# Optimization experiments

Hardware: AMD Instinct MI355X
Metric: run time of the kernel (lower is better)

The kernel has to match this reference:

```python
import jax, jax.numpy as jnp
import numpy as np

B, S, H = 2, 2048, 4096
NH, NKV, HD = 32, 8, 128
Q_SIZE, KV_SIZE = NH * HD, NKV * HD
ROPE_THETA = 10000.0


def setup_inputs() -> dict:
    key = jax.random.key(0)
    k1, k2, k3 = jax.random.split(key, 3)
    positions = jnp.tile(jnp.arange(S, dtype=jnp.int64 if jax.config.jax_enable_x64 else jnp.int32), (B, 1))
    hidden_states = jax.random.normal(k1, (B, S, H), dtype=jnp.float32)
    w_qkv = jax.random.normal(k2, (H, Q_SIZE + 2 * KV_SIZE), dtype=jnp.float32) * 0.02
    w_o = jax.random.normal(k3, (Q_SIZE, H), dtype=jnp.float32) * 0.02
    return {"positions": positions, "hidden_states": hidden_states, "w_qkv": w_qkv, "w_o": w_o}


def _apply_rope(x, positions):
    # x: [B, S, nheads, HD]; neox-style rotate-half RoPE
    half = HD // 2
    inv_freq = 1.0 / (ROPE_THETA ** (jnp.arange(0, half, dtype=jnp.float32) / half))
    freqs = positions.astype(jnp.float32)[..., None] * inv_freq  # [B, S, HD/2]
    cos = jnp.cos(freqs)[:, :, None, :]  # [B, S, 1, HD/2]
    sin = jnp.sin(freqs)[:, :, None, :]
    x1, x2 = x[..., :half], x[..., half:]
    return jnp.concatenate([x1 * cos - x2 * sin, x2 * cos + x1 * sin], axis=-1)


def reference(positions, hidden_states, w_qkv, w_o):
    qkv = jnp.einsum("bsh,hd->bsd", hidden_states, w_qkv)
    q = qkv[..., :Q_SIZE].reshape(B, S, NH, HD)
    k = qkv[..., Q_SIZE:Q_SIZE + KV_SIZE].reshape(B, S, NKV, HD)
    v = qkv[..., Q_SIZE + KV_SIZE:].reshape(B, S, NKV, HD)

    q = _apply_rope(q, positions)
    k = _apply_rope(k, positions)

    # GQA: expand kv heads to match query heads
    rep = NH // NKV
    k = jnp.repeat(k, rep, axis=2)  # [B, S, NH, HD]
    v = jnp.repeat(v, rep, axis=2)

    scale = 1.0 / jnp.sqrt(jnp.float32(HD))
    scores = jnp.einsum("bqhd,bkhd->bhqk", q, k) * scale  # [B, NH, S, S]
    causal = jnp.tril(jnp.ones((S, S), dtype=bool))
    scores = jnp.where(causal[None, None], scores, jnp.finfo(scores.dtype).min)
    probs = jax.nn.softmax(scores, axis=-1)

    attn = jnp.einsum("bhqk,bkhd->bqhd", probs, v).reshape(B, S, Q_SIZE)
    return jnp.einsum("bsd,dh->bsh", attn, w_o)
```

## Files before the change

### kernel.cpp

```cpp
#include <hip/hip_runtime.h>
#include <hip/hip_bf16.h>
#include <math.h>


typedef __attribute__((ext_vector_type(8))) __bf16 bf16x8;
typedef __attribute__((ext_vector_type(4))) float floatx4;

__device__ __forceinline__ floatx4 mfma16(bf16x8 a, bf16x8 b, floatx4 c) {
    return __builtin_amdgcn_mfma_f32_16x16x32_bf16(a, b, c, 0, 0, 0);
}

__device__ __forceinline__ void load_lds16(const __hip_bfloat16* g,
                                           __hip_bfloat16* lds_base_uniform) {
    __builtin_amdgcn_global_load_lds(
        (const __attribute__((address_space(1))) unsigned int*)g,
        (__attribute__((address_space(3))) unsigned int*)lds_base_uniform,
        16, 0, 0);
}

__global__ __launch_bounds__(256)
void convert_kernel(const float* __restrict__ in, __hip_bfloat16* __restrict__ out,
                    int n) {
    int i = (blockIdx.x * 256 + threadIdx.x) * 4;
    if (i >= n) return;
    float4 v = *(const float4*)(in + i);
    union { __hip_bfloat16 h[4]; uint2 u; } pk;
    pk.h[0] = __float2bfloat16(v.x);
    pk.h[1] = __float2bfloat16(v.y);
    pk.h[2] = __float2bfloat16(v.z);
    pk.h[3] = __float2bfloat16(v.w);
    *(uint2*)(out + i) = pk.u;
}

__global__ __launch_bounds__(256)
void transpose_f32_bf16_kernel(const float* __restrict__ in,
                               __hip_bfloat16* __restrict__ out, int R, int C) {
    __shared__ __hip_bfloat16 tile[64][65];
    const int r0 = blockIdx.y * 64, c0 = blockIdx.x * 64;
    const int t = threadIdx.x;
    #pragma unroll
    for (int i = 0; i < 16; ++i) {
        int idx = t + 256 * i;
        int rl = idx >> 6, cl = idx & 63;
        tile[rl][cl] = __float2bfloat16(in[(size_t)(r0 + rl) * C + (c0 + cl)]);
    }
    __syncthreads();
    #pragma unroll
    for (int i = 0; i < 16; ++i) {
        int idx = t + 256 * i;
        int cl = idx >> 6, rl = idx & 63;
        out[(size_t)(c0 + cl) * R + (r0 + rl)] = tile[rl][cl];
    }
}

__global__ __launch_bounds__(256)
void transpose_bf16_kernel(const __hip_bfloat16* __restrict__ in,
                           __hip_bfloat16* __restrict__ out, int R, int C) {
    __shared__ __hip_bfloat16 tile[64][65];
    const int bz = blockIdx.z;
    const __hip_bfloat16* inb  = in  + (size_t)bz * R * C;
    __hip_bfloat16*       outb = out + (size_t)bz * R * C;
    const int r0 = blockIdx.y * 64, c0 = blockIdx.x * 64;
    const int t = threadIdx.x;
    #pragma unroll
    for (int i = 0; i < 16; ++i) {
        int idx = t + 256 * i;
        int rl = idx >> 6, cl = idx & 63;
        tile[rl][cl] = inb[(size_t)(r0 + rl) * C + (c0 + cl)];
    }
    __syncthreads();
    #pragma unroll
    for (int i = 0; i < 16; ++i) {
        int idx = t + 256 * i;
        int cl = idx >> 6, rl = idx & 63;
        outb[(size_t)(c0 + cl) * R + (r0 + rl)] = tile[rl][cl];
    }
}

template <int MODE>
__global__ __launch_bounds__(256)
void gemm_bt_kernel(const __hip_bfloat16* __restrict__ A,
                    const __hip_bfloat16* __restrict__ Bt,
                    float* __restrict__ Cp,
                    __hip_bfloat16* __restrict__ Qr,
                    __hip_bfloat16* __restrict__ Kr,
                    __hip_bfloat16* __restrict__ Vv,
                    int M, int N, int K) {
    __shared__ __align__(16) __hip_bfloat16 As[128 * 32];
    __shared__ __align__(16) __hip_bfloat16 Bs[128 * 32];

    const int m0 = blockIdx.y * 128, n0 = blockIdx.x * 128;
    const int tid  = threadIdx.x;
    const int wave = tid >> 6, lane = tid & 63;
    const int quad = lane >> 4, l16 = lane & 15;
    const int wm = (wave >> 1) * 64, wn = (wave & 1) * 64;

    floatx4 acc[4][4] = {};

    for (int kt = 0; kt < K; kt += 32) {
        #pragma unroll
        for (int i = 0; i < 2; ++i) {
            int idx = tid + 256 * i;
            int row = idx >> 2;
            int kc  = (idx & 3) << 3;
            __hip_bfloat16* dstA = &As[(size_t)(wave * 64 + 256 * i) * 8];
            __hip_bfloat16* dstB = &Bs[(size_t)(wave * 64 + 256 * i) * 8];
            load_lds16(&A [(size_t)(m0 + row) * K + kt + kc], dstA);
            load_lds16(&Bt[(size_t)(n0 + row) * K + kt + kc], dstB);
        }
        __syncthreads();

        bf16x8 af[4], bfv[4];
        #pragma unroll
        for (int i = 0; i < 4; ++i)
            af[i]  = *(const bf16x8*)(&As[(wm + i * 16 + l16) * 32 + quad * 8]);
        #pragma unroll
        for (int j = 0; j < 4; ++j)
            bfv[j] = *(const bf16x8*)(&Bs[(wn + j * 16 + l16) * 32 + quad * 8]);
        #pragma unroll
        for (int i = 0; i < 4; ++i)
            #pragma unroll
            for (int j = 0; j < 4; ++j)
                acc[i][j] = mfma16(af[i], bfv[j], acc[i][j]);
        __syncthreads();
    }

    #pragma unroll
    for (int i = 0; i < 4; ++i) {
        #pragma unroll
        for (int j = 0; j < 4; ++j) {
            int col = n0 + wn + j * 16 + l16;
            #pragma unroll
            for (int r = 0; r < 4; ++r) {
                int row = m0 + wm + i * 16 + quad * 4 + r;
                if (MODE == 0) {
                    Cp[(size_t)row * N + col] = acc[i][j][r];
                } else {
                    __hip_bfloat16 v = __float2bfloat16(acc[i][j][r]);
                    int bb = row >> 11, s = row & 2047;
                    int d  = col & 127;
                    if (col < 4096) {
                        int h = col >> 7;
                        Qr[(((size_t)bb * 32 + h) * 2048 + s) * 128 + d] = v;
                    } else if (col < 5120) {
                        int kvh = (col - 4096) >> 7;
                        Kr[(((size_t)bb * 8 + kvh) * 2048 + s) * 128 + d] = v;
                    } else {
                        int kvh = (col - 5120) >> 7;
                        Vv[(((size_t)bb * 8 + kvh) * 2048 + s) * 128 + d] = v;
                    }
                }
            }
        }
    }
}

__global__ __launch_bounds__(256)
void rope_kernel(__hip_bfloat16* __restrict__ x,
                 const int* __restrict__ positions, int nrows, int bshift,
                 float qscale) {
    int gid = blockIdx.x * 256 + threadIdx.x;
    if (gid >= nrows * 64) return;
    int row = gid >> 6, d = gid & 63;
    int s = row & 2047;
    int b = row >> bshift;
    float p = (float)positions[(b << 11) + s];
    float ang = p * expf(-0.14391156831212787f * (float)d);
    float sn, cs;
    sincosf(ang, &sn, &cs);
    __hip_bfloat16* ptr = x + (size_t)row * 128;
    float x1 = __bfloat162float(ptr[d]);
    float x2 = __bfloat162float(ptr[d + 64]);
    ptr[d]      = __float2bfloat16((x1 * cs - x2 * sn) * qscale);
    ptr[d + 64] = __float2bfloat16((x2 * cs + x1 * sn) * qscale);
}

__global__ __launch_bounds__(256)
void attn_kernel(const __hip_bfloat16* __restrict__ Qr,
                 const __hip_bfloat16* __restrict__ Kr,
                 const __hip_bfloat16* __restrict__ Vt,
                 __hip_bfloat16* __restrict__ Ao) {
    __shared__ __align__(16) __hip_bfloat16 Ks[32 * 136];
    __shared__ __align__(16) __hip_bfloat16 Vs[128 * 36];
    __shared__ __align__(16) __hip_bfloat16 Pl[4][32 * 40];

    const int tid  = threadIdx.x;
    const int wave = tid >> 6, lane = tid & 63;
    const int quad = lane >> 4, l16 = lane & 15;
    const int qb = (gridDim.x - 1) - blockIdx.x;
    const int q0 = qb * 128;
    const int qr0 = q0 + wave * 32;
    const int h  = blockIdx.y;
    const int b  = blockIdx.z;
    const int kv = h >> 2;

    const __hip_bfloat16* Qb = Qr + ((size_t)b * 32 + h)  * 2048 * 128;
    const __hip_bfloat16* Kb = Kr + ((size_t)b * 8  + kv) * 2048 * 128;
    const __hip_bfloat16* Vb = Vt + ((size_t)b * 8  + kv) * 128 * 2048;

    bf16x8 qf[2][4];
    #pragma unroll
    for (int i = 0; i < 2; ++i)
        #pragma unroll
        for (int kc = 0; kc < 4; ++kc)
            qf[i][kc] = *(const bf16x8*)(
                &Qb[(size_t)(qr0 + i * 16 + l16) * 128 + kc * 32 + quad * 8]);

    float m_i[2][4];
    #pragma unroll
    for (int i = 0; i < 2; ++i)
        #pragma unroll
        for (int r = 0; r < 4; ++r) m_i[i][r] = -1e30f;
    floatx4 o[2][8] = {};
    floatx4 lsum[2] = {};

    bf16x8 ones;
    #pragma unroll
    for (int e = 0; e < 8; ++e) ones[e] = (__bf16)1.0f;

    const int kmax = q0 + 127;

    for (int ks = 0; ks <= kmax; ks += 32) {
        #pragma unroll
        for (int p = 0; p < 2; ++p) {
            int idx = tid + 256 * p;
            int krow = idx >> 4, kcol = (idx & 15) << 3;
            *(uint4*)(&Ks[krow * 136 + kcol]) =
                *(const uint4*)(&Kb[(size_t)(ks + krow) * 128 + kcol]);
        }
        #pragma unroll
        for (int p = 0; p < 2; ++p) {
            int idx = tid + 256 * p;
            int d = idx >> 2, koff = (idx & 3) << 3;
            *(uint4*)(&Vs[d * 36 + koff]) =
                *(const uint4*)(&Vb[(size_t)d * 2048 + ks + koff]);
        }
        __syncthreads();

        if (ks <= qr0 + 31) {
            const bool fullt = (ks + 31 <= qr0);

            floatx4 sacc[2][2] = {};
            __builtin_amdgcn_s_setprio(1);
            #pragma unroll
            for (int j = 0; j < 2; ++j) {
                #pragma unroll
                for (int kc = 0; kc < 4; ++kc) {
                    bf16x8 kf = *(const bf16x8*)(
                        &Ks[(j * 16 + l16) * 136 + kc * 32 + quad * 8]);
                    #pragma unroll
                    for (int i = 0; i < 2; ++i)
                        sacc[i][j] = mfma16(qf[i][kc], kf, sacc[i][j]);
                }
            }
            __builtin_amdgcn_s_setprio(0);

            #pragma unroll
            for (int i = 0; i < 2; ++i) {
                #pragma unroll
                for (int r = 0; r < 4; ++r) {
                    int row = qr0 + i * 16 + quad * 4 + r;
                    float s0 = sacc[i][0][r];
                    float s1 = sacc[i][1][r];
                    if (!fullt) {
                        if (ks + l16 > row)      s0 = -1e30f;
                        if (ks + 16 + l16 > row) s1 = -1e30f;
                    }
                    float mx = fmaxf(s0, s1);
                    #pragma unroll
                    for (int off = 1; off < 16; off <<= 1)
                        mx = fmaxf(mx, __shfl_xor(mx, off, 64));
                    float mnew = fmaxf(m_i[i][r], mx);
                    float a  = __expf(m_i[i][r] - mnew);
                    float p0 = __expf(s0 - mnew);
                    float p1 = __expf(s1 - mnew);
                    Pl[wave][(i * 16 + quad * 4 + r) * 40 + l16]      =
                        __float2bfloat16(p0);
                    Pl[wave][(i * 16 + quad * 4 + r) * 40 + 16 + l16] =
                        __float2bfloat16(p1);
                    m_i[i][r] = mnew;
                    lsum[i][r] *= a;
                    #pragma unroll
                    for (int dn = 0; dn < 8; ++dn)
                        o[i][dn][r] *= a;
                }
            }

            bf16x8 pf[2];
            #pragma unroll
            for (int i = 0; i < 2; ++i)
                pf[i] = *(const bf16x8*)(&Pl[wave][(i * 16 + l16) * 40 + quad * 8]);

            __builtin_amdgcn_s_setprio(1);
            #pragma unroll
            for (int i = 0; i < 2; ++i)
                lsum[i] = mfma16(pf[i], ones, lsum[i]);
            #pragma unroll
            for (int dn = 0; dn < 8; ++dn) {
                bf16x8 vf = *(const bf16x8*)(
                    &Vs[(dn * 16 + l16) * 36 + quad * 8]);
                #pragma unroll
                for (int i = 0; i < 2; ++i)
                    o[i][dn] = mfma16(pf[i], vf, o[i][dn]);
            }
            __builtin_amdgcn_s_setprio(0);
        }
        __syncthreads();
    }

    #pragma unroll
    for (int i = 0; i < 2; ++i) {
        #pragma unroll
        for (int r = 0; r < 4; ++r) {
            float inv = 1.0f / lsum[i][r];
            int row = qr0 + i * 16 + quad * 4 + r;
            size_t base = ((size_t)b * 2048 + row) * 4096 + (size_t)h * 128;
            #pragma unroll
            for (int dn = 0; dn < 8; ++dn)
                Ao[base + dn * 16 + l16] = __float2bfloat16(o[i][dn][r] * inv);
        }
    }
}

extern "C" void kernel_launch(void* const* d_in, const int* in_sizes, int n_in,
                              void* d_out, int out_size, void* d_ws, size_t ws_size,
                              hipStream_t stream) {
    const int*   positions = (const int*)d_in[0];
    const float* hidden    = (const float*)d_in[1];
    const float* wqkv      = (const float*)d_in[2];
    const float* wo        = (const float*)d_in[3];
    float* out = (float*)d_out;

    __hip_bfloat16* WqkvT = (__hip_bfloat16*)d_ws;
    __hip_bfloat16* WoT   = WqkvT + 25165824;
    __hip_bfloat16* Hb    = WoT   + 16777216;
    __hip_bfloat16* Qr    = Hb    + 16777216;
    __hip_bfloat16* Kr    = Qr    + 16777216;
    __hip_bfloat16* Vv    = Kr    + 4194304;
    __hip_bfloat16* Ao    = WqkvT;
    __hip_bfloat16* Vt    = Hb;

    convert_kernel<<<16777216 / 1024, 256, 0, stream>>>(hidden, Hb, 16777216);
    transpose_f32_bf16_kernel<<<dim3(6144 / 64, 4096 / 64), 256, 0, stream>>>(
        wqkv, WqkvT, 4096, 6144);
    transpose_f32_bf16_kernel<<<dim3(4096 / 64, 4096 / 64), 256, 0, stream>>>(
        wo, WoT, 4096, 4096);

    gemm_bt_kernel<1><<<dim3(6144 / 128, 4096 / 128), 256, 0, stream>>>(
        Hb, WqkvT, nullptr, Qr, Kr, Vv, 4096, 6144, 4096);

    rope_kernel<<<(131072 * 64) / 256, 256, 0, stream>>>(
        Qr, positions, 131072, 16, 0.08838834764831845f);
    rope_kernel<<<(32768  * 64) / 256, 256, 0, stream>>>(
        Kr, positions, 32768, 14, 1.0f);

    transpose_bf16_kernel<<<dim3(128 / 64, 2048 / 64, 16), 256, 0, stream>>>(
        Vv, Vt, 2048, 128);

    attn_kernel<<<dim3(2048 / 128, 32, 2), 256, 0, stream>>>(Qr, Kr, Vt, Ao);

    gemm_bt_kernel<0><<<dim3(4096 / 128, 4096 / 128), 256, 0, stream>>>(
        Ao, WoT, out, nullptr, nullptr, nullptr, 4096, 4096, 4096);
}
```

Measured before the change: 1.082 ms.

## Double-buffer K/V tiles via async global-to-LDS loads with XOR swizzle

The attention kernel now stages K and V tiles into two LDS buffers using direct global_load_lds, prefetching the next tile while the current one is computed. This replaces the synchronous register round-trip and the barrier before each tile. Padding is swapped for XOR swizzles on K, V and P to avoid LDS bank conflicts. Query-block ordering is also alternated across heads to balance the causal workload. The change relies on a single barrier per iteration being enough to order the async LDS writes against reads of the other buffer.

```diff
diff --git a/kernel.cpp b/kernel.cpp
--- a/kernel.cpp
+++ b/kernel.cpp
@@ -175,19 +175,37 @@
     ptr[d + 64] = __float2bfloat16((x2 * cs + x1 * sn) * qscale);
 }
 
+__device__ __forceinline__ void stage_tiles(const __hip_bfloat16* __restrict__ Kb,
+                                            const __hip_bfloat16* __restrict__ Vb,
+                                            int ks,
+                                            __hip_bfloat16* KsBuf,
+                                            __hip_bfloat16* VsBuf,
+                                            int tid, int wave) {
+    #pragma unroll
+    for (int p = 0; p < 2; ++p) {
+        int idx  = tid + 256 * p;
+        int krow = idx >> 4, kc16 = idx & 15;
+        load_lds16(&Kb[(size_t)(ks + krow) * 128 + ((kc16 ^ (krow & 7)) << 3)],
+                   &KsBuf[(wave * 64 + 256 * p) * 8]);
+        int vrow = idx >> 2, vc16 = idx & 3;
+        load_lds16(&Vb[(size_t)vrow * 2048 + ks + ((vc16 ^ (vrow & 3)) << 3)],
+                   &VsBuf[(wave * 64 + 256 * p) * 8]);
+    }
+}
+
 __global__ __launch_bounds__(256)
 void attn_kernel(const __hip_bfloat16* __restrict__ Qr,
                  const __hip_bfloat16* __restrict__ Kr,
                  const __hip_bfloat16* __restrict__ Vt,
                  __hip_bfloat16* __restrict__ Ao) {
-    __shared__ __align__(16) __hip_bfloat16 Ks[32 * 136];
-    __shared__ __align__(16) __hip_bfloat16 Vs[128 * 36];
-    __shared__ __align__(16) __hip_bfloat16 Pl[4][32 * 40];
+    __shared__ __align__(16) __hip_bfloat16 Ks[2][32 * 128];
+    __shared__ __align__(16) __hip_bfloat16 Vs[2][128 * 32];
+    __shared__ __align__(16) __hip_bfloat16 Pl[4][32 * 32];
 
     const int tid  = threadIdx.x;
     const int wave = tid >> 6, lane = tid & 63;
     const int quad = lane >> 4, l16 = lane & 15;
-    const int qb = (gridDim.x - 1) - blockIdx.x;
+    const int qb = (blockIdx.y & 16) ? blockIdx.x : (15 - blockIdx.x);
     const int q0 = qb * 128;
     const int qr0 = q0 + wave * 32;
     const int h  = blockIdx.y;
@@ -218,26 +236,21 @@
     #pragma unroll
     for (int e = 0; e < 8; ++e) ones[e] = (__bf16)1.0f;
 
-    const int kmax = q0 + 127;
-
-    for (int ks = 0; ks <= kmax; ks += 32) {
-        #pragma unroll
-        for (int p = 0; p < 2; ++p) {
-            int idx = tid + 256 * p;
-            int krow = idx >> 4, kcol = (idx & 15) << 3;
-            *(uint4*)(&Ks[krow * 136 + kcol]) =
-                *(const uint4*)(&Kb[(size_t)(ks + krow) * 128 + kcol]);
-        }
-        #pragma unroll
-        for (int p = 0; p < 2; ++p) {
-            int idx = tid + 256 * p;
-            int d = idx >> 2, koff = (idx & 3) << 3;
-            *(uint4*)(&Vs[d * 36 + koff]) =
-                *(const uint4*)(&Vb[(size_t)d * 2048 + ks + koff]);
-        }
-        __syncthreads();
+    const int ntiles = (q0 >> 5) + 4;
+
+    stage_tiles(Kb, Vb, 0, Ks[0], Vs[0], tid, wave);
+    __syncthreads();
+
+    int cur = 0;
+    for (int t = 0; t < ntiles; ++t) {
+        const int ks = t << 5;
+
+        if (t + 1 < ntiles)
+            stage_tiles(Kb, Vb, ks + 32, Ks[cur ^ 1], Vs[cur ^ 1], tid, wave);
 
         if (ks <= qr0 + 31) {
+            const __hip_bfloat16* Kc = Ks[cur];
+            const __hip_bfloat16* Vc = Vs[cur];
             const bool fullt = (ks + 31 <= qr0);
 
             floatx4 sacc[2][2] = {};
@@ -247,7 +260,8 @@
                 #pragma unroll
                 for (int kc = 0; kc < 4; ++kc) {
                     bf16x8 kf = *(const bf16x8*)(
-                        &Ks[(j * 16 + l16) * 136 + kc * 32 + quad * 8]);
+                        &Kc[(j * 16 + l16) * 128 +
+                            (((kc * 4 + quad) ^ (l16 & 7)) << 3)]);
                     #pragma unroll
                     for (int i = 0; i < 2; ++i)
                         sacc[i][j] = mfma16(qf[i][kc], kf, sacc[i][j]);
@@ -274,9 +288,10 @@
                     float a  = __expf(m_i[i][r] - mnew);
                     float p0 = __expf(s0 - mnew);
                     float p1 = __expf(s1 - mnew);
-                    Pl[wave][(i * 16 + quad * 4 + r) * 40 + l16]      =
+                    int prow = i * 16 + quad * 4 + r;
+                    Pl[wave][prow * 32 + (((l16 >> 3) ^ r) << 3) + (l16 & 7)] =
                         __float2bfloat16(p0);
-                    Pl[wave][(i * 16 + quad * 4 + r) * 40 + 16 + l16] =
+                    Pl[wave][prow * 32 + (((2 + (l16 >> 3)) ^ r) << 3) + (l16 & 7)] =
                         __float2bfloat16(p1);
                     m_i[i][r] = mnew;
                     lsum[i][r] *= a;
@@ -289,7 +304,8 @@
             bf16x8 pf[2];
             #pragma unroll
             for (int i = 0; i < 2; ++i)
-                pf[i] = *(const bf16x8*)(&Pl[wave][(i * 16 + l16) * 40 + quad * 8]);
+                pf[i] = *(const bf16x8*)(
+                    &Pl[wave][(i * 16 + l16) * 32 + ((quad ^ (l16 & 3)) << 3)]);
 
             __builtin_amdgcn_s_setprio(1);
             #pragma unroll
@@ -298,7 +314,7 @@
             #pragma unroll
             for (int dn = 0; dn < 8; ++dn) {
                 bf16x8 vf = *(const bf16x8*)(
-                    &Vs[(dn * 16 + l16) * 36 + quad * 8]);
+                    &Vc[(dn * 16 + l16) * 32 + ((quad ^ (l16 & 3)) << 3)]);
                 #pragma unroll
                 for (int i = 0; i < 2; ++i)
                     o[i][dn] = mfma16(pf[i], vf, o[i][dn]);
@@ -306,6 +322,7 @@
             __builtin_amdgcn_s_setprio(0);
         }
         __syncthreads();
+        cur ^= 1;
     }
 
     #pragma unroll
```

Result: faster. 1.011 ms (-6.5%).
